# Kernel tuning notes

Hardware: AMD Instinct MI355X
Metric: run time of the kernel (lower is better)

## Reference

```python
import jax, jax.numpy as jnp
import numpy as np

VOCAB = 50000
EMB = 100
BATCH = 2048
CTX = 10


def setup_inputs() -> dict:
    key = jax.random.key(0)
    k1, k2, k3, k4 = jax.random.split(key, 4)
    x_positive = jax.random.randint(k1, (BATCH, CTX), 0, VOCAB)
    y = jax.random.randint(k2, (BATCH,), 0, VOCAB)
    emb_v = jax.random.normal(k3, (VOCAB, EMB), dtype=jnp.float32)
    emb_u = jax.random.normal(k4, (VOCAB, EMB), dtype=jnp.float32)
    return {"x_positive": x_positive, "y": y, "emb_v": emb_v, "emb_u": emb_u}


def reference(x_positive, y, emb_v, emb_u):
    # h: mean of context embeddings, [B, E]
    h = emb_v[x_positive].mean(axis=1)
    # positive score: dot(emb_u[y], h) per row -> -logsigmoid
    pos = -jax.nn.log_sigmoid(jnp.einsum("be,be->b", emb_u[y], h))
    # negative score: (-U) @ h for every vocab word -> sigmoid -> sum over vocab -> log
    neg_scores = -jnp.einsum("be,ve->bv", h, emb_u)  # [B, V]
    neg = jnp.log(jax.nn.sigmoid(neg_scores).sum(axis=1))
    return jnp.mean(pos + neg)
```

## Files before the change

kernel.cpp:

```cpp
#include <hip/hip_runtime.h>
#include <math.h>

#define VOCAB 50000
#define VPAD  50048
#define EMB   100
#define BATCH 2048
#define CTX   10

#define NVT   391
#define BC    4
#define PROWS (2 * NVT)

#define CVTB  (VPAD / 16)
#define HB    1024


typedef __attribute__((ext_vector_type(8))) short short8;
typedef __attribute__((ext_vector_type(4))) float f32x4;

__device__ __forceinline__ unsigned short f2bf(float x) {
    union { float f; unsigned u; } v; v.f = x;
    unsigned r = (v.u + 0x7FFFu + ((v.u >> 16) & 1u)) >> 16;
    return (unsigned short)r;
}

__global__ __launch_bounds__(256)
void k_prep(const float* __restrict__ u, unsigned short* __restrict__ ubf,
            const int* __restrict__ x, const float* __restrict__ emb_v,
            float* __restrict__ hf, unsigned short* __restrict__ hbf,
            float* __restrict__ out) {
    const int blk = blockIdx.x;
    const int t   = threadIdx.x;
    if (blk < CVTB) {
        const int r0  = blk * 16;
        const int c16 = t & 15;
        const int fc  = t >> 4;
        const int kc  = fc >> 2, q = fc & 3;
        const int row = r0 + c16;
        const int e   = kc * 32 + q * 8;
        short8 o = (short8)(short)0;
        if (row < VOCAB) {
            if (e + 8 <= EMB) {
                const float4 a = *(const float4*)&u[row * EMB + e];
                const float4 b = *(const float4*)&u[row * EMB + e + 4];
                o[0] = (short)f2bf(a.x); o[1] = (short)f2bf(a.y);
                o[2] = (short)f2bf(a.z); o[3] = (short)f2bf(a.w);
                o[4] = (short)f2bf(b.x); o[5] = (short)f2bf(b.y);
                o[6] = (short)f2bf(b.z); o[7] = (short)f2bf(b.w);
            } else if (e < EMB) {
                const float4 a = *(const float4*)&u[row * EMB + e];
                o[0] = (short)f2bf(a.x); o[1] = (short)f2bf(a.y);
                o[2] = (short)f2bf(a.z); o[3] = (short)f2bf(a.w);
            }
        }
        const int tile = r0 >> 7, mg = (r0 >> 4) & 7;
        *(short8*)&ubf[(size_t)tile * 16384 + (size_t)mg * 2048 + t * 8] = o;
    } else {
        const int b = (blk - CVTB) * 2 + (t >> 7);
        const int e = t & 127;
        if (blk == CVTB && t == 0) out[0] = 0.0f;
        float s = 0.0f;
        if (e < EMB) {
#pragma unroll
            for (int c = 0; c < CTX; ++c) {
                const int idx = x[b * CTX + c];
                s += emb_v[idx * EMB + e];
            }
            s *= (1.0f / CTX);
            hf[b * EMB + e] = s;
        }
        const int kc = e >> 5, q = (e >> 3) & 3, j = e & 7;
        hbf[(b >> 4) * 2048 + (kc * 64 + q * 16 + (b & 15)) * 8 + j] =
            (e < EMB) ? f2bf(s) : (unsigned short)0;
    }
}

__global__ __launch_bounds__(256, 4)
void k_neg(const unsigned short* __restrict__ hbf, const unsigned short* __restrict__ ubf,
           float* __restrict__ partial) {
    __shared__ unsigned short us[16384];

    const int t   = threadIdx.x;
    const int w   = t >> 6;
    const int L   = t & 63;
    const int wvh = w & 1;
    const int wbh = w >> 1;
    const int vy  = blockIdx.y;

    const unsigned short* src = ubf + (size_t)vy * 16384;
#pragma unroll
    for (int i = 0; i < 8; ++i)
        *(short8*)&us[(i * 256 + t) * 8] = *(const short8*)&src[(i * 256 + t) * 8];
    __syncthreads();

    short8 af01[2][4];
#pragma unroll
    for (int kc = 0; kc < 2; ++kc)
#pragma unroll
        for (int mi = 0; mi < 4; ++mi)
            af01[kc][mi] = *(const short8*)&us[(((wvh * 4 + mi) * 4 + kc) * 64 + L) * 8];

    const int b0base = blockIdx.x * (BATCH / BC);
    const int prow   = (2 * vy + wvh) * BATCH;

#pragma unroll 1
    for (int bt = 0; bt < 8; ++bt) {
        const int Bg0 = (b0base + bt * 64) >> 4;

        f32x4 acc[4][2];
#pragma unroll
        for (int mi = 0; mi < 4; ++mi)
#pragma unroll
            for (int ni = 0; ni < 2; ++ni) acc[mi][ni] = (f32x4)(0.0f);

#pragma unroll
        for (int kc = 0; kc < 4; ++kc) {
            short8 bf[2];
#pragma unroll
            for (int ni = 0; ni < 2; ++ni)
                bf[ni] = *(const short8*)&hbf[(size_t)(Bg0 + wbh * 2 + ni) * 2048 + (kc * 64 + L) * 8];
#pragma unroll
            for (int mi = 0; mi < 4; ++mi) {
                const short8 af = (kc < 2)
                    ? af01[kc][mi]
                    : *(const short8*)&us[(((wvh * 4 + mi) * 4 + kc) * 64 + L) * 8];
#pragma unroll
                for (int ni = 0; ni < 2; ++ni)
                    acc[mi][ni] = __builtin_amdgcn_mfma_f32_16x16x32_bf16(
                        af, bf[ni], acc[mi][ni], 0, 0, 0);
            }
        }

#pragma unroll
        for (int ni = 0; ni < 2; ++ni) {
            float p = 0.0f;
#pragma unroll
            for (int mi = 0; mi < 4; ++mi) {
                const float ea = __expf(acc[mi][ni][0]);
                const float eb = __expf(acc[mi][ni][1]);
                const float ec = __expf(acc[mi][ni][2]);
                const float ed = __expf(acc[mi][ni][3]);
                const float n1 = 2.0f + ea + eb;
                const float d1 = fmaf(ea, eb, n1 - 1.0f);
                const float n2 = 2.0f + ec + ed;
                const float d2 = fmaf(ec, ed, n2 - 1.0f);
                const float N  = fmaf(n1, d2, n2 * d1);
                p = fmaf(N, __builtin_amdgcn_rcpf(d1 * d2), p);
            }
            p += __shfl_down(p, 32);
            p += __shfl_down(p, 16);
            if (L < 16)
                partial[prow + b0base + bt * 64 + wbh * 32 + ni * 16 + L] = p;
        }
    }
}

__global__ void k_redfinal(const int* __restrict__ y, const float* __restrict__ hf,
                           const float* __restrict__ u, const float* __restrict__ partial,
                           float* __restrict__ out) {
    const int t    = threadIdx.x;
    const int lane = t & 63;
    const int w    = t >> 6;
    const int b    = blockIdx.x * 64 + lane;
    float s = 0.0f;
    for (int r = w; r < PROWS; r += 16)
        s += partial[r * BATCH + b];
    __shared__ float red[16][64];
    red[w][lane] = s;
    __syncthreads();
    if (w == 0) {
        float ns = -(float)(VPAD - VOCAB) * 0.5f;
#pragma unroll
        for (int i = 0; i < 16; ++i) ns += red[i][lane];

        const int yi = y[b];
        const float4* hp = (const float4*)&hf[b * EMB];
        const float4* up = (const float4*)&u[yi * EMB];
        float dot = 0.0f;
#pragma unroll
        for (int qq = 0; qq < EMB / 4; ++qq) {
            const float4 a = hp[qq];
            const float4 c = up[qq];
            dot += a.x * c.x + a.y * c.y + a.z * c.z + a.w * c.w;
        }
        const float pos = fmaxf(-dot, 0.0f) + log1pf(__expf(-fabsf(dot)));
        float val = pos + logf(ns);
#pragma unroll
        for (int off = 32; off; off >>= 1) val += __shfl_down(val, off, 64);
        if (lane == 0) atomicAdd(out, val * (1.0f / BATCH));
    }
}

extern "C" void kernel_launch(void* const* d_in, const int* in_sizes, int n_in,
                              void* d_out, int out_size, void* d_ws, size_t ws_size,
                              hipStream_t stream) {
    const int*   x     = (const int*)d_in[0];
    const int*   y     = (const int*)d_in[1];
    const float* emb_v = (const float*)d_in[2];
    const float* emb_u = (const float*)d_in[3];
    float* out = (float*)d_out;

    float*          hf      = (float*)d_ws;
    float*          partial = hf + BATCH * EMB;
    unsigned short* hbf     = (unsigned short*)(partial + PROWS * BATCH);
    unsigned short* ubf     = hbf + BATCH * 128;

    k_prep    <<<dim3(CVTB + HB), dim3(256), 0, stream>>>(emb_u, ubf, x, emb_v, hf, hbf, out);
    k_neg     <<<dim3(BC, NVT), dim3(256), 0, stream>>>(hbf, ubf, partial);
    k_redfinal<<<dim3(BATCH / 64), dim3(1024), 0, stream>>>(y, hf, emb_u, partial, out);
}
```

Baseline: 143.0 us.

## Switch negative-score GEMM from bf16 to fp8 with scaled 16x16x128 MFMA

Converts emb_u and h to FP8 (e4m3 via cvt_pk_fp8) instead of bf16, lays them out for the 16x16x128 f8f6f4 scaled MFMA, and covers the whole K=128 in one instruction per tile. The A fragments now load straight from global memory into registers, with no LDS staging or barrier. Batch splitting doubles from 4 to 8 chunks for more blocks. This cuts memory traffic and MFMA count, but FP8 precision inside exp/sigmoid sums over 50k words may add error to the result.

```diff
diff --git a/kernel.cpp b/kernel.cpp
--- a/kernel.cpp
+++ b/kernel.cpp
@@ -8,53 +8,49 @@
 #define CTX   10
 
 #define NVT   391
-#define BC    4
+#define BC    8
 #define PROWS (2 * NVT)
-
-#define CVTB  (VPAD / 16)
-#define HB    1024
+#define NMG   (VPAD / 16)
+#define CVTB  (NMG / 4)
+#define HBLK  (BATCH / 2)
 
 
-typedef __attribute__((ext_vector_type(8))) short short8;
+typedef __attribute__((ext_vector_type(8))) int   i32x8;
 typedef __attribute__((ext_vector_type(4))) float f32x4;
 
-__device__ __forceinline__ unsigned short f2bf(float x) {
-    union { float f; unsigned u; } v; v.f = x;
-    unsigned r = (v.u + 0x7FFFu + ((v.u >> 16) & 1u)) >> 16;
-    return (unsigned short)r;
-}
-
 __global__ __launch_bounds__(256)
-void k_prep(const float* __restrict__ u, unsigned short* __restrict__ ubf,
+void k_prep(const float* __restrict__ u, unsigned char* __restrict__ ub8,
             const int* __restrict__ x, const float* __restrict__ emb_v,
-            float* __restrict__ hf, unsigned short* __restrict__ hbf,
+            float* __restrict__ hf, unsigned char* __restrict__ hb8,
             float* __restrict__ out) {
     const int blk = blockIdx.x;
     const int t   = threadIdx.x;
     if (blk < CVTB) {
-        const int r0  = blk * 16;
-        const int c16 = t & 15;
-        const int fc  = t >> 4;
-        const int kc  = fc >> 2, q = fc & 3;
-        const int row = r0 + c16;
-        const int e   = kc * 32 + q * 8;
-        short8 o = (short8)(short)0;
+        const int mgid = blk * 4 + (t >> 6);
+        const int L    = t & 63;
+        const int c16  = L & 15;
+        const int q    = L >> 4;
+        const int row  = mgid * 16 + c16;
+        const int e0   = q * 32;
+        i32x8 o = (i32x8)0;
         if (row < VOCAB) {
-            if (e + 8 <= EMB) {
-                const float4 a = *(const float4*)&u[row * EMB + e];
-                const float4 b = *(const float4*)&u[row * EMB + e + 4];
-                o[0] = (short)f2bf(a.x); o[1] = (short)f2bf(a.y);
-                o[2] = (short)f2bf(a.z); o[3] = (short)f2bf(a.w);
-                o[4] = (short)f2bf(b.x); o[5] = (short)f2bf(b.y);
-                o[6] = (short)f2bf(b.z); o[7] = (short)f2bf(b.w);
-            } else if (e < EMB) {
-                const float4 a = *(const float4*)&u[row * EMB + e];
-                o[0] = (short)f2bf(a.x); o[1] = (short)f2bf(a.y);
-                o[2] = (short)f2bf(a.z); o[3] = (short)f2bf(a.w);
+            if (q < 3) {
+                const float4* p = (const float4*)&u[row * EMB + e0];
+#pragma unroll
+                for (int j = 0; j < 8; ++j) {
+                    const float4 v = p[j];
+                    int wd = __builtin_amdgcn_cvt_pk_fp8_f32(v.x, v.y, 0, false);
+                    wd     = __builtin_amdgcn_cvt_pk_fp8_f32(v.z, v.w, wd, true);
+                    o[j] = wd;
+                }
+            } else {
+                const float4 v = *(const float4*)&u[row * EMB + 96];
+                int wd = __builtin_amdgcn_cvt_pk_fp8_f32(v.x, v.y, 0, false);
+                wd     = __builtin_amdgcn_cvt_pk_fp8_f32(v.z, v.w, wd, true);
+                o[0] = wd;
             }
         }
-        const int tile = r0 >> 7, mg = (r0 >> 4) & 7;
-        *(short8*)&ubf[(size_t)tile * 16384 + (size_t)mg * 2048 + t * 8] = o;
+        *(i32x8*)&ub8[((size_t)mgid * 64 + L) * 32] = o;
     } else {
         const int b = (blk - CVTB) * 2 + (t >> 7);
         const int e = t & 127;
@@ -69,17 +65,15 @@
             s *= (1.0f / CTX);
             hf[b * EMB + e] = s;
         }
-        const int kc = e >> 5, q = (e >> 3) & 3, j = e & 7;
-        hbf[(b >> 4) * 2048 + (kc * 64 + q * 16 + (b & 15)) * 8 + j] =
-            (e < EMB) ? f2bf(s) : (unsigned short)0;
+        const unsigned char f8 =
+            (unsigned char)(__builtin_amdgcn_cvt_pk_fp8_f32(s, 0.0f, 0, false) & 0xFF);
+        hb8[((b >> 4) * 64 + (e >> 5) * 16 + (b & 15)) * 32 + (e & 31)] = f8;
     }
 }
 
 __global__ __launch_bounds__(256, 4)
-void k_neg(const unsigned short* __restrict__ hbf, const unsigned short* __restrict__ ubf,
+void k_neg(const unsigned char* __restrict__ hb8, const unsigned char* __restrict__ ub8,
            float* __restrict__ partial) {
-    __shared__ unsigned short us[16384];
-
     const int t   = threadIdx.x;
     const int w   = t >> 6;
     const int L   = t & 63;
@@ -87,25 +81,23 @@
     const int wbh = w >> 1;
     const int vy  = blockIdx.y;
 
-    const unsigned short* src = ubf + (size_t)vy * 16384;
+    i32x8 af[4];
 #pragma unroll
-    for (int i = 0; i < 8; ++i)
-        *(short8*)&us[(i * 256 + t) * 8] = *(const short8*)&src[(i * 256 + t) * 8];
-    __syncthreads();
-
-    short8 af01[2][4];
-#pragma unroll
-    for (int kc = 0; kc < 2; ++kc)
-#pragma unroll
-        for (int mi = 0; mi < 4; ++mi)
-            af01[kc][mi] = *(const short8*)&us[(((wvh * 4 + mi) * 4 + kc) * 64 + L) * 8];
+    for (int mi = 0; mi < 4; ++mi)
+        af[mi] = *(const i32x8*)&ub8[(((size_t)vy * 8 + wvh * 4 + mi) * 64 + L) * 32];
 
     const int b0base = blockIdx.x * (BATCH / BC);
     const int prow   = (2 * vy + wvh) * BATCH;
 
 #pragma unroll 1
-    for (int bt = 0; bt < 8; ++bt) {
-        const int Bg0 = (b0base + bt * 64) >> 4;
+    for (int bt = 0; bt < (BATCH / BC) / 64; ++bt) {
+        const int b0  = b0base + bt * 64;
+        const int Bg0 = b0 >> 4;
+
+        i32x8 bf[2];
+#pragma unroll
+        for (int ni = 0; ni < 2; ++ni)
+            bf[ni] = *(const i32x8*)&hb8[((size_t)(Bg0 + wbh * 2 + ni) * 64 + L) * 32];
 
         f32x4 acc[4][2];
 #pragma unroll
@@ -114,22 +106,14 @@
             for (int ni = 0; ni < 2; ++ni) acc[mi][ni] = (f32x4)(0.0f);
 
 #pragma unroll
-        for (int kc = 0; kc < 4; ++kc) {
-            short8 bf[2];
+        for (int mi = 0; mi < 4; ++mi)
 #pragma unroll
             for (int ni = 0; ni < 2; ++ni)
-                bf[ni] = *(const short8*)&hbf[(size_t)(Bg0 + wbh * 2 + ni) * 2048 + (kc * 64 + L) * 8];
-#pragma unroll
-            for (int mi = 0; mi < 4; ++mi) {
-                const short8 af = (kc < 2)
-                    ? af01[kc][mi]
-                    : *(const short8*)&us[(((wvh * 4 + mi) * 4 + kc) * 64 + L) * 8];
-#pragma unroll
-                for (int ni = 0; ni < 2; ++ni)
-                    acc[mi][ni] = __builtin_amdgcn_mfma_f32_16x16x32_bf16(
-                        af, bf[ni], acc[mi][ni], 0, 0, 0);
-            }
-        }
+                acc[mi][ni] = __builtin_amdgcn_mfma_scale_f32_16x16x128_f8f6f4(
+                    af[mi], bf[ni], acc[mi][ni],
+                    0, 0,
+                    0, 0x7F7F7F7F,
+                    0, 0x7F7F7F7F);
 
 #pragma unroll
         for (int ni = 0; ni < 2; ++ni) {
@@ -150,7 +134,7 @@
             p += __shfl_down(p, 32);
             p += __shfl_down(p, 16);
             if (L < 16)
-                partial[prow + b0base + bt * 64 + wbh * 32 + ni * 16 + L] = p;
+                partial[prow + b0 + wbh * 32 + ni * 16 + L] = p;
         }
     }
 }
@@ -200,12 +184,12 @@
     const float* emb_u = (const float*)d_in[3];
     float* out = (float*)d_out;
 
-    float*          hf      = (float*)d_ws;
-    float*          partial = hf + BATCH * EMB;
-    unsigned short* hbf     = (unsigned short*)(partial + PROWS * BATCH);
-    unsigned short* ubf     = hbf + BATCH * 128;
+    float*         hf      = (float*)d_ws;
+    float*         partial = hf + BATCH * EMB;
+    unsigned char* hb8     = (unsigned char*)(partial + PROWS * BATCH);
+    unsigned char* ub8     = hb8 + (size_t)(BATCH / 16) * 2048;
 
-    k_prep    <<<dim3(CVTB + HB), dim3(256), 0, stream>>>(emb_u, ubf, x, emb_v, hf, hbf, out);
-    k_neg     <<<dim3(BC, NVT), dim3(256), 0, stream>>>(hbf, ubf, partial);
+    k_prep    <<<dim3(CVTB + HBLK), dim3(256), 0, stream>>>(emb_u, ub8, x, emb_v, hf, hb8, out);
+    k_neg     <<<dim3(BC, NVT), dim3(256), 0, stream>>>(hb8, ub8, partial);
     k_redfinal<<<dim3(BATCH / 64), dim3(1024), 0, stream>>>(y, hf, emb_u, partial, out);
 }
```

Measured after the change: 131.2 us. -8.3%, faster.
